# Performance work log

Measured on AMD Instinct MI355X. Metric: run time of the kernel, lower is better.

The kernel has to match this reference:

```python
import jax, jax.numpy as jnp
import numpy as np

N = 50000
E = 800000
IN_DIM = 128
HID = 64
HEADS = 4
OUT_DIM = 64
NEG_SLOPE = 0.2


def setup_inputs() -> dict:
    key = jax.random.key(0)
    ks = jax.random.split(key, 10)
    x = jax.random.normal(ks[0], (N, IN_DIM), dtype=jnp.float32)
    edge_index = jax.random.randint(ks[1], (2, E), 0, N, dtype=jnp.int64)
    s1 = 1.0 / np.sqrt(IN_DIM)
    s2 = 1.0 / np.sqrt(HEADS * HID)
    return {
        "x": x,
        "edge_index": edge_index,
        "W1": jax.random.normal(ks[2], (IN_DIM, HEADS * HID), dtype=jnp.float32) * s1,
        "a_src1": jax.random.normal(ks[3], (HEADS, HID), dtype=jnp.float32) * s2,
        "a_dst1": jax.random.normal(ks[4], (HEADS, HID), dtype=jnp.float32) * s2,
        "b1": jnp.zeros((HEADS * HID,), dtype=jnp.float32),
        "W2": jax.random.normal(ks[5], (HEADS * HID, OUT_DIM), dtype=jnp.float32) * s2,
        "a_src2": jax.random.normal(ks[6], (1, OUT_DIM), dtype=jnp.float32) * 0.125,
        "a_dst2": jax.random.normal(ks[7], (1, OUT_DIM), dtype=jnp.float32) * 0.125,
        "b2": jnp.zeros((OUT_DIM,), dtype=jnp.float32),
    }


def gat_layer(x, src, dst, W, a_src, a_dst, bias, heads, ch, concat):
    n = x.shape[0]
    h = (x @ W).reshape(n, heads, ch)                      # [N,H,C]
    asrc = jnp.einsum('nhc,hc->nh', h, a_src)              # [N,H]
    adst = jnp.einsum('nhc,hc->nh', h, a_dst)              # [N,H]
    e = asrc[src] + adst[dst]                              # [E',H]
    e = jnp.where(e > 0, e, NEG_SLOPE * e)                 # LeakyReLU(0.2)
    # segment softmax over incoming edges of each dst node
    m = jax.ops.segment_max(e, dst, num_segments=n)        # [N,H]
    m = jnp.where(jnp.isfinite(m), m, 0.0)
    ex = jnp.exp(e - m[dst])
    denom = jax.ops.segment_sum(ex, dst, num_segments=n)   # [N,H]
    alpha = ex / (denom[dst] + 1e-16)                      # [E',H]
    out = jax.ops.segment_sum(alpha[:, :, None] * h[src], dst, num_segments=n)  # [N,H,C]
    if concat:
        out = out.reshape(n, heads * ch)
    else:
        out = out.mean(axis=1)
    return out + bias


def reference(x, edge_index, W1, a_src1, a_dst1, b1, W2, a_src2, a_dst2, b2):
    n = x.shape[0]
    loops = jnp.arange(n, dtype=edge_index.dtype)
    src = jnp.concatenate([edge_index[0], loops])          # add self-loops (PyG default)
    dst = jnp.concatenate([edge_index[1], loops])
    h = gat_layer(x, src, dst, W1, a_src1, a_dst1, b1, HEADS, HID, True)
    h = jax.nn.elu(h)
    out = gat_layer(h, src, dst, W2, a_src2, a_dst2, b2, 1, OUT_DIM, False)
    return out
```

## Files before the change

### kernel.cpp

```cpp
#include <hip/hip_runtime.h>
#include <hip/hip_bf16.h>

#define NN 50000
#define EE 800000
#define IN_DIM 128
#define HH 256
#define HID 64
#define HEADS 4
#define OUT_DIM 64
#define SCAN_BLOCKS 196
#define G1_BLOCKS 782
#define SCAT_BLOCKS 3125
#define AGG_BLOCKS 3125
#define TOTW (AGG_BLOCKS * 4)

static __device__ __forceinline__ unsigned short f2bf(float f) {
    unsigned int u = __float_as_uint(f);
    u += 0x7fffu + ((u >> 16) & 1u);
    return (unsigned short)(u >> 16);
}
static __device__ __forceinline__ float bf2f(unsigned short h) {
    return __uint_as_float(((unsigned int)h) << 16);
}


__global__ void hist_kernel(const int* __restrict__ ei, int* __restrict__ deg) {
    int e = blockIdx.x * 256 + threadIdx.x;
    atomicAdd(&deg[ei[EE + e]], 1);
}

__global__ __launch_bounds__(256) void block_scan_kernel(
    const int* __restrict__ deg, int* __restrict__ local_scan,
    int* __restrict__ block_sum) {
    __shared__ int tmp[256];
    int t = threadIdx.x, i = blockIdx.x * 256 + t;
    int v = (i < NN) ? deg[i] : 0;
    tmp[t] = v;
    __syncthreads();
    for (int d = 1; d < 256; d <<= 1) {
        int u = (t >= d) ? tmp[t - d] : 0;
        __syncthreads();
        tmp[t] += u;
        __syncthreads();
    }
    if (i < NN) local_scan[i] = tmp[t] - v;
    if (t == 255) block_sum[blockIdx.x] = tmp[255];
}

__global__ __launch_bounds__(256) void scan_sums_kernel(int* __restrict__ block_sum) {
    __shared__ int tmp[256];
    int t = threadIdx.x;
    int v = (t < SCAN_BLOCKS) ? block_sum[t] : 0;
    tmp[t] = v;
    __syncthreads();
    for (int d = 1; d < 256; d <<= 1) {
        int u = (t >= d) ? tmp[t - d] : 0;
        __syncthreads();
        tmp[t] += u;
        __syncthreads();
    }
    if (t < SCAN_BLOCKS) block_sum[t] = tmp[t] - v;
}

__global__ __launch_bounds__(256) void finalize_kernel(
    const int* __restrict__ local_scan, const int* __restrict__ block_sum,
    int* __restrict__ row_ptr, int* __restrict__ cursor) {
    int i = blockIdx.x * 256 + threadIdx.x;
    if (i < NN) {
        int v = local_scan[i] + block_sum[blockIdx.x];
        row_ptr[i] = v; cursor[i] = v;
    }
    if (i == 0) row_ptr[NN] = EE;
}


__global__ __launch_bounds__(256) void gemm1_scatter_kernel(
    const float* __restrict__ x, const float* __restrict__ W1,
    const float* __restrict__ a_src1, const float* __restrict__ a_dst1,
    unsigned short* __restrict__ h1, float* __restrict__ asrc1, float* __restrict__ adst1,
    const int* __restrict__ ei, int* __restrict__ cursor, int* __restrict__ edge_src) {
    if (blockIdx.x >= G1_BLOCKS) {
        int e = (blockIdx.x - G1_BLOCKS) * 256 + threadIdx.x;
        int d = ei[EE + e];
        int pos = atomicAdd(&cursor[d], 1);
        edge_src[pos] = ei[e];
        return;
    }
    __shared__ __align__(16) float xs[64][IN_DIM];
    int t = threadIdx.x;
    int row0 = blockIdx.x * 64;
    #pragma unroll
    for (int j = 0; j < 8; j++) {
        int idx = t + j * 256;
        int r = idx >> 5, k4 = (idx & 31) * 4;
        int rr = row0 + r; if (rr >= NN) rr = NN - 1;
        *reinterpret_cast<float4*>(&xs[r][k4]) =
            *reinterpret_cast<const float4*>(&x[(size_t)rr * IN_DIM + k4]);
    }
    __syncthreads();
    int lane = t & 63, wid = t >> 6;
    float4 acc[16];
    #pragma unroll
    for (int r = 0; r < 16; r++) acc[r] = make_float4(0.f, 0.f, 0.f, 0.f);
    const float* wbase = W1 + lane * 4;
    for (int k = 0; k < IN_DIM; k += 4) {
        float4 w0 = *reinterpret_cast<const float4*>(&wbase[(k + 0) * HH]);
        float4 w1 = *reinterpret_cast<const float4*>(&wbase[(k + 1) * HH]);
        float4 w2 = *reinterpret_cast<const float4*>(&wbase[(k + 2) * HH]);
        float4 w3 = *reinterpret_cast<const float4*>(&wbase[(k + 3) * HH]);
        #pragma unroll
        for (int r = 0; r < 16; r++) {
            float4 xv = *reinterpret_cast<const float4*>(&xs[wid * 16 + r][k]);
            acc[r].x = fmaf(xv.x, w0.x, acc[r].x); acc[r].y = fmaf(xv.x, w0.y, acc[r].y);
            acc[r].z = fmaf(xv.x, w0.z, acc[r].z); acc[r].w = fmaf(xv.x, w0.w, acc[r].w);
            acc[r].x = fmaf(xv.y, w1.x, acc[r].x); acc[r].y = fmaf(xv.y, w1.y, acc[r].y);
            acc[r].z = fmaf(xv.y, w1.z, acc[r].z); acc[r].w = fmaf(xv.y, w1.w, acc[r].w);
            acc[r].x = fmaf(xv.z, w2.x, acc[r].x); acc[r].y = fmaf(xv.z, w2.y, acc[r].y);
            acc[r].z = fmaf(xv.z, w2.z, acc[r].z); acc[r].w = fmaf(xv.z, w2.w, acc[r].w);
            acc[r].x = fmaf(xv.w, w3.x, acc[r].x); acc[r].y = fmaf(xv.w, w3.y, acc[r].y);
            acc[r].z = fmaf(xv.w, w3.z, acc[r].z); acc[r].w = fmaf(xv.w, w3.w, acc[r].w);
        }
    }
    float4 asv = *reinterpret_cast<const float4*>(&a_src1[lane * 4]);
    float4 adv = *reinterpret_cast<const float4*>(&a_dst1[lane * 4]);
    int head = lane >> 4;
    #pragma unroll
    for (int r = 0; r < 16; r++) {
        int row = row0 + wid * 16 + r;
        bool ok = row < NN;
        if (ok) {
            ushort4 hv;
            hv.x = f2bf(acc[r].x); hv.y = f2bf(acc[r].y);
            hv.z = f2bf(acc[r].z); hv.w = f2bf(acc[r].w);
            *reinterpret_cast<ushort4*>(&h1[(size_t)row * HH + lane * 4]) = hv;
        }
        float vs = acc[r].x * asv.x + acc[r].y * asv.y + acc[r].z * asv.z + acc[r].w * asv.w;
        float vd = acc[r].x * adv.x + acc[r].y * adv.y + acc[r].z * adv.z + acc[r].w * adv.w;
        #pragma unroll
        for (int o = 1; o < 16; o <<= 1) { vs += __shfl_xor(vs, o); vd += __shfl_xor(vd, o); }
        if (ok && (lane & 15) == 0) {
            asrc1[row * HEADS + head] = vs;
            adst1[row * HEADS + head] = vd;
        }
    }
}


__global__ __launch_bounds__(256) void agg1_kernel(
    const int* __restrict__ row_ptr, const int* __restrict__ edge_src,
    const unsigned short* __restrict__ h1, const float* __restrict__ asrc1,
    const float* __restrict__ adst1, const float* __restrict__ b1,
    float* __restrict__ x2) {
    int wid = threadIdx.x >> 6, lane = threadIdx.x & 63;
    int gw = blockIdx.x * 4 + wid;
    int head = lane >> 4;
    unsigned cb = lane * 4;
    const unsigned short* h1l = h1 + cb;
    const float* asl = asrc1 + head;
    float4 bv = *reinterpret_cast<const float4*>(&b1[cb]);
    for (int node = gw; node < NN; node += TOTW) {
        float ad = adst1[node * HEADS + head];
        int beg = row_ptr[node], end = row_ptr[node + 1];
        float denom = 0.f;
        float ax = 0.f, ay = 0.f, az = 0.f, aw = 0.f;
        int s0 = (beg < end) ? edge_src[beg] : node;
        int s1 = (beg + 1 < end) ? edge_src[beg + 1] : node;
        int s2 = (beg + 2 < end) ? edge_src[beg + 2] : node;
        float e0 = asl[(unsigned)s0 * HEADS];
        float e1 = asl[(unsigned)s1 * HEADS];
        float e2 = asl[(unsigned)s2 * HEADS];
        ushort4 h0 = *reinterpret_cast<const ushort4*>(&h1l[(unsigned)s0 * HH]);
        ushort4 h1v = *reinterpret_cast<const ushort4*>(&h1l[(unsigned)s1 * HH]);
        ushort4 h2v = *reinterpret_cast<const ushort4*>(&h1l[(unsigned)s2 * HH]);
        for (int i = beg; i <= end; i++) {
            int j = i + 3;
            int s3 = (j < end) ? edge_src[j] : node;
            float e3 = asl[(unsigned)s3 * HEADS];
            ushort4 h3 = *reinterpret_cast<const ushort4*>(&h1l[(unsigned)s3 * HH]);
            float e = e0 + ad;
            e = fmaxf(e, 0.2f * e);
            float ex = __expf(e);
            denom += ex;
            ax = fmaf(ex, bf2f(h0.x), ax); ay = fmaf(ex, bf2f(h0.y), ay);
            az = fmaf(ex, bf2f(h0.z), az); aw = fmaf(ex, bf2f(h0.w), aw);
            e0 = e1; h0 = h1v;
            e1 = e2; h1v = h2v;
            e2 = e3; h2v = h3;
        }
        float inv = 1.0f / (denom + 1e-16f);
        float v0 = ax * inv + bv.x;
        float v1 = ay * inv + bv.y;
        float v2 = az * inv + bv.z;
        float v3 = aw * inv + bv.w;
        v0 = v0 > 0.f ? v0 : (__expf(v0) - 1.f);
        v1 = v1 > 0.f ? v1 : (__expf(v1) - 1.f);
        v2 = v2 > 0.f ? v2 : (__expf(v2) - 1.f);
        v3 = v3 > 0.f ? v3 : (__expf(v3) - 1.f);
        float4 o; o.x = v0; o.y = v1; o.z = v2; o.w = v3;
        *reinterpret_cast<float4*>(&x2[(size_t)node * HH + cb]) = o;
    }
}


__global__ __launch_bounds__(256) void gemm2_kernel(
    const float* __restrict__ x2, const float* __restrict__ W2,
    const float* __restrict__ a_src2, const float* __restrict__ a_dst2,
    unsigned short* __restrict__ h2, float* __restrict__ asrc2, float* __restrict__ adst2) {
    __shared__ __align__(16) float xs[32][HH];
    int t = threadIdx.x;
    int row0 = blockIdx.x * 32;
    #pragma unroll
    for (int j = 0; j < 8; j++) {
        int idx = t + j * 256;
        int r = idx >> 6, k4 = (idx & 63) * 4;
        int rr = row0 + r; if (rr >= NN) rr = NN - 1;
        *reinterpret_cast<float4*>(&xs[r][k4]) =
            *reinterpret_cast<const float4*>(&x2[(size_t)rr * HH + k4]);
    }
    __syncthreads();
    int c = t & 63, wid = t >> 6;
    float acc[8];
    #pragma unroll
    for (int r = 0; r < 8; r++) acc[r] = 0.f;
    for (int k = 0; k < HH; k += 4) {
        float w0 = W2[(k + 0) * OUT_DIM + c];
        float w1 = W2[(k + 1) * OUT_DIM + c];
        float w2 = W2[(k + 2) * OUT_DIM + c];
        float w3 = W2[(k + 3) * OUT_DIM + c];
        #pragma unroll
        for (int r = 0; r < 8; r++) {
            float4 xv = *reinterpret_cast<const float4*>(&xs[wid * 8 + r][k]);
            acc[r] = fmaf(xv.x, w0, acc[r]);
            acc[r] = fmaf(xv.y, w1, acc[r]);
            acc[r] = fmaf(xv.z, w2, acc[r]);
            acc[r] = fmaf(xv.w, w3, acc[r]);
        }
    }
    float as = a_src2[c], ad = a_dst2[c];
    #pragma unroll
    for (int r = 0; r < 8; r++) {
        int row = row0 + wid * 8 + r;
        bool ok = row < NN;
        if (ok) h2[(size_t)row * OUT_DIM + c] = f2bf(acc[r]);
        float vs = acc[r] * as, vd = acc[r] * ad;
        #pragma unroll
        for (int o = 32; o > 0; o >>= 1) { vs += __shfl_xor(vs, o); vd += __shfl_xor(vd, o); }
        if (ok && c == 0) { asrc2[row] = vs; adst2[row] = vd; }
    }
}


__global__ __launch_bounds__(256) void agg2_kernel(
    const int* __restrict__ row_ptr, const int* __restrict__ edge_src,
    const unsigned short* __restrict__ h2, const float* __restrict__ asrc2,
    const float* __restrict__ adst2, const float* __restrict__ b2,
    float* __restrict__ out) {
    int wid = threadIdx.x >> 6, lane = threadIdx.x & 63;
    int gw = blockIdx.x * 4 + wid;
    const unsigned short* h2l = h2 + lane;
    float bl = b2[lane];
    for (int node = gw; node < NN; node += TOTW) {
        float ad = adst2[node];
        int beg = row_ptr[node], end = row_ptr[node + 1];
        float denom = 0.f, acc = 0.f;
        int s0 = (beg < end) ? edge_src[beg] : node;
        int s1 = (beg + 1 < end) ? edge_src[beg + 1] : node;
        int s2 = (beg + 2 < end) ? edge_src[beg + 2] : node;
        float e0 = asrc2[s0], e1 = asrc2[s1], e2 = asrc2[s2];
        unsigned short h0 = h2l[(unsigned)s0 * OUT_DIM];
        unsigned short h1v = h2l[(unsigned)s1 * OUT_DIM];
        unsigned short h2v = h2l[(unsigned)s2 * OUT_DIM];
        for (int i = beg; i <= end; i++) {
            int j = i + 3;
            int s3 = (j < end) ? edge_src[j] : node;
            float e3 = asrc2[s3];
            unsigned short h3 = h2l[(unsigned)s3 * OUT_DIM];
            float e = e0 + ad;
            e = fmaxf(e, 0.2f * e);
            float ex = __expf(e);
            denom += ex;
            acc = fmaf(ex, bf2f(h0), acc);
            e0 = e1; h0 = h1v;
            e1 = e2; h1v = h2v;
            e2 = e3; h2v = h3;
        }
        out[(size_t)node * OUT_DIM + lane] = acc / (denom + 1e-16f) + bl;
    }
}


extern "C" void kernel_launch(void* const* d_in, const int* in_sizes, int n_in,
                              void* d_out, int out_size, void* d_ws, size_t ws_size,
                              hipStream_t stream) {
    const float* x   = (const float*)d_in[0];
    const int*   ei  = (const int*)d_in[1];
    const float* W1  = (const float*)d_in[2];
    const float* as1 = (const float*)d_in[3];
    const float* ad1 = (const float*)d_in[4];
    const float* b1  = (const float*)d_in[5];
    const float* W2  = (const float*)d_in[6];
    const float* as2 = (const float*)d_in[7];
    const float* ad2 = (const float*)d_in[8];
    const float* b2  = (const float*)d_in[9];
    float* out = (float*)d_out;

    char* ws = (char*)d_ws;
    size_t off = 0;
    auto alloc = [&](size_t bytes) -> void* {
        void* p = ws + off;
        off += (bytes + 255) & ~(size_t)255;
        return p;
    };
    unsigned short* h1 = (unsigned short*)alloc((size_t)NN * HH * 2);
    float* x2     = (float*)alloc((size_t)NN * HH * 4);
    unsigned short* h2 = (unsigned short*)alloc((size_t)NN * OUT_DIM * 2);
    float* asrc1  = (float*)alloc((size_t)NN * HEADS * 4);
    float* adst1  = (float*)alloc((size_t)NN * HEADS * 4);
    float* asrc2  = (float*)alloc((size_t)NN * 4);
    float* adst2  = (float*)alloc((size_t)NN * 4);
    int*   deg    = (int*)alloc((size_t)NN * 4);
    int*   row_ptr= (int*)alloc((size_t)(NN + 1) * 4);
    int*   cursor = (int*)alloc((size_t)NN * 4);
    int*   edge_src=(int*)alloc((size_t)EE * 4);
    int*   local_scan = (int*)alloc((size_t)NN * 4);
    int*   block_sum  = (int*)alloc((size_t)SCAN_BLOCKS * 4);

    hipMemsetAsync(deg, 0, (size_t)NN * 4, stream);
    hist_kernel<<<EE / 256, 256, 0, stream>>>(ei, deg);
    block_scan_kernel<<<SCAN_BLOCKS, 256, 0, stream>>>(deg, local_scan, block_sum);
    scan_sums_kernel<<<1, 256, 0, stream>>>(block_sum);
    finalize_kernel<<<SCAN_BLOCKS, 256, 0, stream>>>(local_scan, block_sum, row_ptr, cursor);
    gemm1_scatter_kernel<<<G1_BLOCKS + SCAT_BLOCKS, 256, 0, stream>>>(
        x, W1, as1, ad1, h1, asrc1, adst1, ei, cursor, edge_src);

    agg1_kernel<<<AGG_BLOCKS, 256, 0, stream>>>(row_ptr, edge_src, h1, asrc1, adst1, b1, x2);
    gemm2_kernel<<<(NN + 31) / 32, 256, 0, stream>>>(x2, W2, as2, ad2, h2, asrc2, adst2);
    agg2_kernel<<<AGG_BLOCKS, 256, 0, stream>>>(row_ptr, edge_src, h2, asrc2, adst2, b2, out);
}
```

Baseline: 392.1 us.

## Store layer-1 output in bf16, prefetch weights, split gemm1 from scatter

The intermediate x2 activation between agg1 and gemm2 is now stored as bf16 instead of fp32, halving its write and read traffic. The weight loads in both GEMM kernels are software-prefetched one k-step ahead to hide global load latency. The fused gemm1+scatter kernel is split back into two separate launches, which removes branch divergence across blocks but adds a launch and loses the overlap between the two. The bf16 storage adds rounding error to the layer-2 input.

```diff
diff --git a/kernel.cpp b/kernel.cpp
--- a/kernel.cpp
+++ b/kernel.cpp
@@ -10,7 +10,6 @@
 #define OUT_DIM 64
 #define SCAN_BLOCKS 196
 #define G1_BLOCKS 782
-#define SCAT_BLOCKS 3125
 #define AGG_BLOCKS 3125
 #define TOTW (AGG_BLOCKS * 4)
 
@@ -73,19 +72,19 @@
     if (i == 0) row_ptr[NN] = EE;
 }
 
-
-__global__ __launch_bounds__(256) void gemm1_scatter_kernel(
+__global__ void scatter_kernel(const int* __restrict__ ei, int* __restrict__ cursor,
+                               int* __restrict__ edge_src) {
+    int e = blockIdx.x * 256 + threadIdx.x;
+    int d = ei[EE + e];
+    int pos = atomicAdd(&cursor[d], 1);
+    edge_src[pos] = ei[e];
+}
+
+
+__global__ __launch_bounds__(256) void gemm1_kernel(
     const float* __restrict__ x, const float* __restrict__ W1,
     const float* __restrict__ a_src1, const float* __restrict__ a_dst1,
-    unsigned short* __restrict__ h1, float* __restrict__ asrc1, float* __restrict__ adst1,
-    const int* __restrict__ ei, int* __restrict__ cursor, int* __restrict__ edge_src) {
-    if (blockIdx.x >= G1_BLOCKS) {
-        int e = (blockIdx.x - G1_BLOCKS) * 256 + threadIdx.x;
-        int d = ei[EE + e];
-        int pos = atomicAdd(&cursor[d], 1);
-        edge_src[pos] = ei[e];
-        return;
-    }
+    unsigned short* __restrict__ h1, float* __restrict__ asrc1, float* __restrict__ adst1) {
     __shared__ __align__(16) float xs[64][IN_DIM];
     int t = threadIdx.x;
     int row0 = blockIdx.x * 64;
@@ -103,11 +102,16 @@
     #pragma unroll
     for (int r = 0; r < 16; r++) acc[r] = make_float4(0.f, 0.f, 0.f, 0.f);
     const float* wbase = W1 + lane * 4;
+    float4 w0 = *reinterpret_cast<const float4*>(&wbase[0 * HH]);
+    float4 w1 = *reinterpret_cast<const float4*>(&wbase[1 * HH]);
+    float4 w2 = *reinterpret_cast<const float4*>(&wbase[2 * HH]);
+    float4 w3 = *reinterpret_cast<const float4*>(&wbase[3 * HH]);
     for (int k = 0; k < IN_DIM; k += 4) {
-        float4 w0 = *reinterpret_cast<const float4*>(&wbase[(k + 0) * HH]);
-        float4 w1 = *reinterpret_cast<const float4*>(&wbase[(k + 1) * HH]);
-        float4 w2 = *reinterpret_cast<const float4*>(&wbase[(k + 2) * HH]);
-        float4 w3 = *reinterpret_cast<const float4*>(&wbase[(k + 3) * HH]);
+        int kn = (k + 4) & 127;
+        float4 nw0 = *reinterpret_cast<const float4*>(&wbase[(kn + 0) * HH]);
+        float4 nw1 = *reinterpret_cast<const float4*>(&wbase[(kn + 1) * HH]);
+        float4 nw2 = *reinterpret_cast<const float4*>(&wbase[(kn + 2) * HH]);
+        float4 nw3 = *reinterpret_cast<const float4*>(&wbase[(kn + 3) * HH]);
         #pragma unroll
         for (int r = 0; r < 16; r++) {
             float4 xv = *reinterpret_cast<const float4*>(&xs[wid * 16 + r][k]);
@@ -120,6 +124,7 @@
             acc[r].x = fmaf(xv.w, w3.x, acc[r].x); acc[r].y = fmaf(xv.w, w3.y, acc[r].y);
             acc[r].z = fmaf(xv.w, w3.z, acc[r].z); acc[r].w = fmaf(xv.w, w3.w, acc[r].w);
         }
+        w0 = nw0; w1 = nw1; w2 = nw2; w3 = nw3;
     }
     float4 asv = *reinterpret_cast<const float4*>(&a_src1[lane * 4]);
     float4 adv = *reinterpret_cast<const float4*>(&a_dst1[lane * 4]);
@@ -150,7 +155,7 @@
     const int* __restrict__ row_ptr, const int* __restrict__ edge_src,
     const unsigned short* __restrict__ h1, const float* __restrict__ asrc1,
     const float* __restrict__ adst1, const float* __restrict__ b1,
-    float* __restrict__ x2) {
+    unsigned short* __restrict__ x2) {
     int wid = threadIdx.x >> 6, lane = threadIdx.x & 63;
     int gw = blockIdx.x * 4 + wid;
     int head = lane >> 4;
@@ -196,14 +201,15 @@
         v1 = v1 > 0.f ? v1 : (__expf(v1) - 1.f);
         v2 = v2 > 0.f ? v2 : (__expf(v2) - 1.f);
         v3 = v3 > 0.f ? v3 : (__expf(v3) - 1.f);
-        float4 o; o.x = v0; o.y = v1; o.z = v2; o.w = v3;
-        *reinterpret_cast<float4*>(&x2[(size_t)node * HH + cb]) = o;
+        ushort4 o;
+        o.x = f2bf(v0); o.y = f2bf(v1); o.z = f2bf(v2); o.w = f2bf(v3);
+        *reinterpret_cast<ushort4*>(&x2[(size_t)node * HH + cb]) = o;
     }
 }
 
 
 __global__ __launch_bounds__(256) void gemm2_kernel(
-    const float* __restrict__ x2, const float* __restrict__ W2,
+    const unsigned short* __restrict__ x2, const float* __restrict__ W2,
     const float* __restrict__ a_src2, const float* __restrict__ a_dst2,
     unsigned short* __restrict__ h2, float* __restrict__ asrc2, float* __restrict__ adst2) {
     __shared__ __align__(16) float xs[32][HH];
@@ -214,19 +220,27 @@
         int idx = t + j * 256;
         int r = idx >> 6, k4 = (idx & 63) * 4;
         int rr = row0 + r; if (rr >= NN) rr = NN - 1;
-        *reinterpret_cast<float4*>(&xs[r][k4]) =
-            *reinterpret_cast<const float4*>(&x2[(size_t)rr * HH + k4]);
+        ushort4 uv = *reinterpret_cast<const ushort4*>(&x2[(size_t)rr * HH + k4]);
+        float4 fv;
+        fv.x = bf2f(uv.x); fv.y = bf2f(uv.y); fv.z = bf2f(uv.z); fv.w = bf2f(uv.w);
+        *reinterpret_cast<float4*>(&xs[r][k4]) = fv;
     }
     __syncthreads();
     int c = t & 63, wid = t >> 6;
     float acc[8];
     #pragma unroll
     for (int r = 0; r < 8; r++) acc[r] = 0.f;
+    const float* wbase = W2 + c;
+    float w0 = wbase[0 * OUT_DIM];
+    float w1 = wbase[1 * OUT_DIM];
+    float w2 = wbase[2 * OUT_DIM];
+    float w3 = wbase[3 * OUT_DIM];
     for (int k = 0; k < HH; k += 4) {
-        float w0 = W2[(k + 0) * OUT_DIM + c];
-        float w1 = W2[(k + 1) * OUT_DIM + c];
-        float w2 = W2[(k + 2) * OUT_DIM + c];
-        float w3 = W2[(k + 3) * OUT_DIM + c];
+        int kn = (k + 4) & 255;
+        float nw0 = wbase[(kn + 0) * OUT_DIM];
+        float nw1 = wbase[(kn + 1) * OUT_DIM];
+        float nw2 = wbase[(kn + 2) * OUT_DIM];
+        float nw3 = wbase[(kn + 3) * OUT_DIM];
         #pragma unroll
         for (int r = 0; r < 8; r++) {
             float4 xv = *reinterpret_cast<const float4*>(&xs[wid * 8 + r][k]);
@@ -235,6 +249,7 @@
             acc[r] = fmaf(xv.z, w2, acc[r]);
             acc[r] = fmaf(xv.w, w3, acc[r]);
         }
+        w0 = nw0; w1 = nw1; w2 = nw2; w3 = nw3;
     }
     float as = a_src2[c], ad = a_dst2[c];
     #pragma unroll
@@ -312,7 +327,7 @@
         return p;
     };
     unsigned short* h1 = (unsigned short*)alloc((size_t)NN * HH * 2);
-    float* x2     = (float*)alloc((size_t)NN * HH * 4);
+    unsigned short* x2 = (unsigned short*)alloc((size_t)NN * HH * 2);
     unsigned short* h2 = (unsigned short*)alloc((size_t)NN * OUT_DIM * 2);
     float* asrc1  = (float*)alloc((size_t)NN * HEADS * 4);
     float* adst1  = (float*)alloc((size_t)NN * HEADS * 4);
@@ -330,8 +345,8 @@
     block_scan_kernel<<<SCAN_BLOCKS, 256, 0, stream>>>(deg, local_scan, block_sum);
     scan_sums_kernel<<<1, 256, 0, stream>>>(block_sum);
     finalize_kernel<<<SCAN_BLOCKS, 256, 0, stream>>>(local_scan, block_sum, row_ptr, cursor);
-    gemm1_scatter_kernel<<<G1_BLOCKS + SCAT_BLOCKS, 256, 0, stream>>>(
-        x, W1, as1, ad1, h1, asrc1, adst1, ei, cursor, edge_src);
+    gemm1_kernel<<<G1_BLOCKS, 256, 0, stream>>>(x, W1, as1, ad1, h1, asrc1, adst1);
+    scatter_kernel<<<EE / 256, 256, 0, stream>>>(ei, cursor, edge_src);
 
     agg1_kernel<<<AGG_BLOCKS, 256, 0, stream>>>(row_ptr, edge_src, h1, asrc1, adst1, b1, x2);
     gemm2_kernel<<<(NN + 31) / 32, 256, 0, stream>>>(x2, W2, as2, ad2, h2, asrc2, adst2);
```

New measurement: 418.1 us. +6.6%, slower.
